# Optimization experiments

Hardware: AMD Instinct MI355X
Metric: run time of the kernel (lower is better)

## Reference

```python
import jax, jax.numpy as jnp
import numpy as np

N_NODES = 100000
N_EDGES = 1600000


def gcn_layer(x, src, dst, W, b, n_nodes):
    # PyG GCNConv: h = x @ W; add self-loops; sym-normalized scatter-add; + bias
    h = x @ W
    loop = jnp.arange(n_nodes, dtype=src.dtype)
    si = jnp.concatenate([src, loop])
    di = jnp.concatenate([dst, loop])
    deg = jax.ops.segment_sum(jnp.ones(si.shape[0], h.dtype), di, num_segments=n_nodes)
    dinv = jax.lax.rsqrt(deg)  # deg >= 1 due to self-loops
    norm = dinv[si] * dinv[di]              # [E+N]
    msgs = h[si] * norm[:, None]            # gather-scale
    out = jax.ops.segment_sum(msgs, di, num_segments=n_nodes)  # scatter-add
    return out + b


def setup_inputs() -> dict:
    key = jax.random.key(0)
    ks = jax.random.split(key, 8)
    x = jax.random.normal(ks[0], (N_NODES, 8), dtype=jnp.float32)
    edge_index = jax.random.randint(ks[1], (2, N_EDGES), 0, N_NODES, dtype=jnp.int32)
    W1 = jax.random.normal(ks[2], (8, 32), dtype=jnp.float32) * 0.3
    b1 = jax.random.normal(ks[3], (32,), dtype=jnp.float32) * 0.1
    W2 = jax.random.normal(ks[4], (32, 16), dtype=jnp.float32) * 0.2
    b2 = jax.random.normal(ks[5], (16,), dtype=jnp.float32) * 0.1
    Wfc = jax.random.normal(ks[6], (16, 1), dtype=jnp.float32) * 0.25
    bfc = jax.random.normal(ks[7], (1,), dtype=jnp.float32) * 0.1
    return {"x": x, "edge_index": edge_index, "W1": W1, "b1": b1,
            "W2": W2, "b2": b2, "Wfc": Wfc, "bfc": bfc}


def reference(x, edge_index, W1, b1, W2, b2, Wfc, bfc):
    n = x.shape[0]
    src, dst = edge_index[0], edge_index[1]
    h = jax.nn.relu(gcn_layer(x, src, dst, W1, b1, n))
    h = jax.nn.relu(gcn_layer(h, src, dst, W2, b2, n))
    return jax.nn.sigmoid(h @ Wfc + bfc)  # [N, 1]
```

## Files before the change

kernel.cpp:

```cpp
#include <hip/hip_runtime.h>
#include <math.h>

#define N_NODES 100000
#define N_EDGES 1600000

#define NB_SHIFT 7
#define NB 128
#define NBINS 782
#define RCAP 2432
#define BCHUNK 4096
#define BINBLOCKS ((N_EDGES + BCHUNK - 1) / BCHUNK)
#define LCAP 16
#define SPB 8

__device__ __forceinline__ unsigned int pack_bf2(float a, float b) {
    unsigned int ua = __float_as_uint(a), ub = __float_as_uint(b);
    ua += 0x7FFFu + ((ua >> 16) & 1u);
    ub += 0x7FFFu + ((ub >> 16) & 1u);
    return (ua >> 16) | (ub & 0xFFFF0000u);
}
__device__ __forceinline__ float bf_lo(unsigned int u) { return __uint_as_float(u << 16); }
__device__ __forceinline__ float bf_hi(unsigned int u) { return __uint_as_float(u & 0xFFFF0000u); }

__global__ __launch_bounds__(512) void k_bin(const int* __restrict__ src, const int* __restrict__ dst,
                                             int* __restrict__ cnt_tab, int* __restrict__ log,
                                             int* __restrict__ spill_rec, int* __restrict__ spill_bin, int e) {
    __shared__ int lcnt[NBINS];
    __shared__ int lbuf[NBINS * LCAP];
    __shared__ int sp_rec[SPB];
    __shared__ int sp_bin[SPB];
    __shared__ int sp_n;
    int tid = threadIdx.x, blk = blockIdx.x;
    for (int b = tid; b < NBINS; b += 512) lcnt[b] = 0;
    if (tid == 0) sp_n = 0;
    __syncthreads();
    int base = blk * BCHUNK;
    int end = min(base + BCHUNK, e);
    for (int i = base + tid; i < end; i += 512) {
        int d = dst[i], s = src[i];
        int b = d >> NB_SHIFT;
        int rec = (s << NB_SHIFT) | (d & (NB - 1));
        int slot = atomicAdd(&lcnt[b], 1);
        if (slot < LCAP) {
            lbuf[b * LCAP + slot] = rec;
        } else {
            int k = atomicAdd(&sp_n, 1);
            if (k < SPB) { sp_rec[k] = rec; sp_bin[k] = b; }
        }
    }
    __syncthreads();
    for (int b = tid; b < NBINS; b += 512) cnt_tab[blk * NBINS + b] = min(lcnt[b], LCAP);
    int* lrow = log + blk * NBINS * LCAP;
    for (int idx = tid; idx < NBINS * LCAP; idx += 512) lrow[idx] = lbuf[idx];
    if (tid < SPB) {
        int valid = tid < min(sp_n, SPB);
        spill_rec[blk * SPB + tid] = valid ? sp_rec[tid] : 0;
        spill_bin[blk * SPB + tid] = valid ? sp_bin[tid] : -1;
    }
}

__global__ __launch_bounds__(512) void k_sort(const int* __restrict__ cnt_tab, const int* __restrict__ log,
                                              const int* __restrict__ spill_rec, const int* __restrict__ spill_bin,
                                              int* __restrict__ gcur, int* __restrict__ regions,
                                              const float* __restrict__ x, float* __restrict__ dinv,
                                              unsigned int* __restrict__ gxu, int* __restrict__ row_start) {
    __shared__ int ccnt[BINBLOCKS];
    __shared__ int coff[BINBLOCKS];
    __shared__ int wtot[8];
    __shared__ int msum_s;
    __shared__ int sp_take;
    __shared__ int lrec[RCAP];
    __shared__ int lsort[RCAP];
    __shared__ int cnt[NB];
    __shared__ int stt[NB];
    __shared__ int cur[NB];
    __shared__ float di_s[NB];
    int b = blockIdx.x, tid = threadIdx.x;
    int lane = tid & 63, wv = tid >> 6;

    for (int c = tid; c < BINBLOCKS; c += 512) ccnt[c] = cnt_tab[c * NBINS + b];
    if (tid == 0) sp_take = 0;
    if (tid < NB) cnt[tid] = 0;
    __syncthreads();
    int v = (tid < BINBLOCKS) ? ccnt[tid] : 0;
    int s = v;
#pragma unroll
    for (int off = 1; off < 64; off <<= 1) {
        int t = __shfl_up(s, off, 64);
        if (lane >= off) s += t;
    }
    if (lane == 63) wtot[wv] = s;
    __syncthreads();
    if (tid == 0) {
        int acc = 0;
#pragma unroll
        for (int w = 0; w < 8; ++w) { int t = wtot[w]; wtot[w] = acc; acc += t; }
        msum_s = acc;
    }
    __syncthreads();
    if (tid < BINBLOCKS) coff[tid] = (s - v) + wtot[wv];
    __syncthreads();
    for (int idx = tid; idx < BINBLOCKS * LCAP; idx += 512) {
        int c = idx >> 4, k = idx & (LCAP - 1);
        if (k < ccnt[c]) {
            int pos = coff[c] + k;
            if (pos < RCAP) {
                int rec = log[(c * NBINS + b) * LCAP + k];
                lrec[pos] = rec;
                atomicAdd(&cnt[rec & (NB - 1)], 1);
            }
        }
    }
    for (int jj = tid; jj < BINBLOCKS * SPB; jj += 512) {
        if (spill_bin[jj] == b) {
            int p = atomicAdd(&sp_take, 1);
            int pos = msum_s + p;
            if (pos < RCAP) {
                int rec = spill_rec[jj];
                lrec[pos] = rec;
                atomicAdd(&cnt[rec & (NB - 1)], 1);
            }
        }
    }
    __syncthreads();
    int m = min(msum_s + sp_take, RCAP);
    if (tid == 0) gcur[b] = m;
    if (tid < 64) {
        int c0 = cnt[lane], c1 = cnt[64 + lane];
        int s0 = c0, s1 = c1;
#pragma unroll
        for (int off = 1; off < 64; off <<= 1) {
            int t0 = __shfl_up(s0, off, 64);
            int t1 = __shfl_up(s1, off, 64);
            if (lane >= off) { s0 += t0; s1 += t1; }
        }
        s1 += __shfl(s0, 63, 64);
        stt[lane] = s0 - c0;
        stt[64 + lane] = s1 - c1;
    }
    __syncthreads();
    int node0 = b << NB_SHIFT;
    if (tid < NB) {
        cur[tid] = stt[tid];
        float d = rsqrtf((float)cnt[tid] + 1.0f);
        di_s[tid] = d;
        row_start[b * NB + tid] = b * RCAP + stt[tid];
        int node = node0 + tid;
        if (node < N_NODES) dinv[node] = d;
    }
    __syncthreads();
    {
        int l = tid >> 2, p = tid & 3;
        int node = node0 + l;
        if (node < N_NODES) {
            const float2* x2 = (const float2*)x;
            float2 xv = x2[node * 4 + p];
            float d = di_s[l];
            gxu[node * 4 + p] = pack_bf2(xv.x * d, xv.y * d);
        }
    }
    for (int j = tid; j < m; j += 512) {
        int rec = lrec[j];
        int pos = atomicAdd(&cur[rec & (NB - 1)], 1);
        lsort[pos] = rec >> NB_SHIFT;
    }
    __syncthreads();
    int* wb = regions + b * RCAP;
    for (int j = tid; j < m; j += 512) wb[j] = lsort[j];
}

__global__ __launch_bounds__(256) void k_agg1_mlp(const int* __restrict__ gcur, const int* __restrict__ regions,
                                                  const int* __restrict__ row_start,
                                                  const unsigned int* __restrict__ gxu,
                                                  const float* __restrict__ dinv,
                                                  const float* __restrict__ W1, const float* __restrict__ b1,
                                                  const float* __restrict__ W2,
                                                  unsigned int* __restrict__ g2u) {
    int t = blockIdx.x * blockDim.x + threadIdx.x;
    int i = t >> 2;
    if (i >= N_NODES) return;
    int q = t & 3;
    int b = i >> NB_SHIFT, l = i & (NB - 1);
    int js = row_start[i];
    int je = (l < NB - 1) ? row_start[i + 1] : b * RCAP + gcur[b];
    const uint4* gx4 = (const uint4*)gxu;
    float a0 = 0.f, a1 = 0.f, a2 = 0.f, a3 = 0.f, a4 = 0.f, a5 = 0.f, a6 = 0.f, a7 = 0.f;
    if (q == 0) {
        uint4 u = gx4[i];
        a0 = bf_lo(u.x); a1 = bf_hi(u.x); a2 = bf_lo(u.y); a3 = bf_hi(u.y);
        a4 = bf_lo(u.z); a5 = bf_hi(u.z); a6 = bf_lo(u.w); a7 = bf_hi(u.w);
    }
    for (int j = js + q; j < je; j += 4) {
        uint4 u = gx4[regions[j]];
        a0 += bf_lo(u.x); a1 += bf_hi(u.x); a2 += bf_lo(u.y); a3 += bf_hi(u.y);
        a4 += bf_lo(u.z); a5 += bf_hi(u.z); a6 += bf_lo(u.w); a7 += bf_hi(u.w);
    }
    a0 += __shfl_xor(a0, 1, 64); a0 += __shfl_xor(a0, 2, 64);
    a1 += __shfl_xor(a1, 1, 64); a1 += __shfl_xor(a1, 2, 64);
    a2 += __shfl_xor(a2, 1, 64); a2 += __shfl_xor(a2, 2, 64);
    a3 += __shfl_xor(a3, 1, 64); a3 += __shfl_xor(a3, 2, 64);
    a4 += __shfl_xor(a4, 1, 64); a4 += __shfl_xor(a4, 2, 64);
    a5 += __shfl_xor(a5, 1, 64); a5 += __shfl_xor(a5, 2, 64);
    a6 += __shfl_xor(a6, 1, 64); a6 += __shfl_xor(a6, 2, 64);
    a7 += __shfl_xor(a7, 1, 64); a7 += __shfl_xor(a7, 2, 64);
    float di = dinv[i];
    float y[8] = { a0 * di, a1 * di, a2 * di, a3 * di, a4 * di, a5 * di, a6 * di, a7 * di };
    float hh[8];
#pragma unroll
    for (int ff = 0; ff < 8; ++ff) {
        int f = q * 8 + ff;
        float s = b1[f];
#pragma unroll
        for (int k = 0; k < 8; ++k) s += y[k] * W1[k * 32 + f];
        hh[ff] = fmaxf(0.f, s);
    }
    float g[16];
#pragma unroll
    for (int o = 0; o < 16; ++o) {
        float s = 0.f;
#pragma unroll
        for (int ff = 0; ff < 8; ++ff) s += hh[ff] * W2[(q * 8 + ff) * 16 + o];
        g[o] = s;
    }
#pragma unroll
    for (int o = 0; o < 16; ++o) {
        g[o] += __shfl_xor(g[o], 1, 64);
        g[o] += __shfl_xor(g[o], 2, 64);
    }
    int f0 = q * 4;
    uint2 pk = make_uint2(pack_bf2(g[f0] * di, g[f0 + 1] * di),
                          pack_bf2(g[f0 + 2] * di, g[f0 + 3] * di));
    ((uint2*)g2u)[i * 4 + q] = pk;
}

__global__ __launch_bounds__(256) void k_agg2_final(const int* __restrict__ gcur, const int* __restrict__ regions,
                                                    const int* __restrict__ row_start,
                                                    const unsigned int* __restrict__ g2u,
                                                    const float* __restrict__ dinv,
                                                    const float* __restrict__ b2, const float* __restrict__ Wfc,
                                                    const float* __restrict__ bfc, float* __restrict__ out) {
    int t = blockIdx.x * blockDim.x + threadIdx.x;
    int i = t >> 2;
    if (i >= N_NODES) return;
    int q = t & 3;
    int b = i >> NB_SHIFT, l = i & (NB - 1);
    int js = row_start[i];
    int je = (l < NB - 1) ? row_start[i + 1] : b * RCAP + gcur[b];
    const uint4* g24 = (const uint4*)g2u;
    float a[16];
#pragma unroll
    for (int f = 0; f < 16; ++f) a[f] = 0.f;
    if (q == 0) {
        uint4 u0 = g24[i * 2], u1 = g24[i * 2 + 1];
        a[0] = bf_lo(u0.x); a[1] = bf_hi(u0.x); a[2] = bf_lo(u0.y); a[3] = bf_hi(u0.y);
        a[4] = bf_lo(u0.z); a[5] = bf_hi(u0.z); a[6] = bf_lo(u0.w); a[7] = bf_hi(u0.w);
        a[8] = bf_lo(u1.x); a[9] = bf_hi(u1.x); a[10] = bf_lo(u1.y); a[11] = bf_hi(u1.y);
        a[12] = bf_lo(u1.z); a[13] = bf_hi(u1.z); a[14] = bf_lo(u1.w); a[15] = bf_hi(u1.w);
    }
    for (int j = js + q; j < je; j += 4) {
        int s = regions[j];
        uint4 u0 = g24[s * 2], u1 = g24[s * 2 + 1];
        a[0] += bf_lo(u0.x); a[1] += bf_hi(u0.x); a[2] += bf_lo(u0.y); a[3] += bf_hi(u0.y);
        a[4] += bf_lo(u0.z); a[5] += bf_hi(u0.z); a[6] += bf_lo(u0.w); a[7] += bf_hi(u0.w);
        a[8] += bf_lo(u1.x); a[9] += bf_hi(u1.x); a[10] += bf_lo(u1.y); a[11] += bf_hi(u1.y);
        a[12] += bf_lo(u1.z); a[13] += bf_hi(u1.z); a[14] += bf_lo(u1.w); a[15] += bf_hi(u1.w);
    }
#pragma unroll
    for (int f = 0; f < 16; ++f) {
        a[f] += __shfl_xor(a[f], 1, 64);
        a[f] += __shfl_xor(a[f], 2, 64);
    }
    if (q == 0) {
        float di = dinv[i];
        float z = bfc[0];
#pragma unroll
        for (int f = 0; f < 16; ++f)
            z += fmaxf(0.f, di * a[f] + b2[f]) * Wfc[f];
        out[i] = 1.0f / (1.0f + expf(-z));
    }
}

extern "C" void kernel_launch(void* const* d_in, const int* in_sizes, int n_in,
                              void* d_out, int out_size, void* d_ws, size_t ws_size,
                              hipStream_t stream) {
    const float* x   = (const float*)d_in[0];
    const int*   ei  = (const int*)d_in[1];
    const float* W1  = (const float*)d_in[2];
    const float* b1  = (const float*)d_in[3];
    const float* W2  = (const float*)d_in[4];
    const float* b2  = (const float*)d_in[5];
    const float* Wfc = (const float*)d_in[6];
    const float* bfc = (const float*)d_in[7];
    float* out = (float*)d_out;

    const int* src = ei;
    const int* dst = ei + N_EDGES;
    const int N = N_NODES, E = N_EDGES;

    int*          cnt_tab   = (int*)d_ws;
    int*          log       = cnt_tab + BINBLOCKS * NBINS;
    int*          spill_rec = log + BINBLOCKS * NBINS * LCAP;
    int*          spill_bin = spill_rec + BINBLOCKS * SPB;
    int*          gcur      = spill_bin + BINBLOCKS * SPB;
    int*          regions   = gcur + NBINS;
    int*          row_start = regions + NBINS * RCAP;
    float*        dinv      = (float*)(row_start + NBINS * NB);
    unsigned int* gxu       = (unsigned int*)(dinv + N);
    unsigned int* g2u       = gxu + N * 4;

    auto grid = [](int work, int blk) { return (work + blk - 1) / blk; };

    k_bin<<<BINBLOCKS, 512, 0, stream>>>(src, dst, cnt_tab, log, spill_rec, spill_bin, E);
    k_sort<<<NBINS, 512, 0, stream>>>(cnt_tab, log, spill_rec, spill_bin, gcur, regions, x, dinv, gxu, row_start);
    k_agg1_mlp<<<grid(N * 4, 256), 256, 0, stream>>>(gcur, regions, row_start, gxu, dinv, W1, b1, W2, g2u);
    k_agg2_final<<<grid(N * 4, 256), 256, 0, stream>>>(gcur, regions, row_start, g2u, dinv, b2, Wfc, bfc, out);
}
```

Before: 152.0 us.

## Fuse layer-1 aggregation into sort kernel using global degree atomics

```diff
diff --git a/kernel.cpp b/kernel.cpp
--- a/kernel.cpp
+++ b/kernel.cpp
@@ -22,15 +22,30 @@
 __device__ __forceinline__ float bf_lo(unsigned int u) { return __uint_as_float(u << 16); }
 __device__ __forceinline__ float bf_hi(unsigned int u) { return __uint_as_float(u & 0xFFFF0000u); }
 
+#define QR(v) { v += __shfl_xor(v, 1, 64); v += __shfl_xor(v, 2, 64); }
+
 __global__ __launch_bounds__(512) void k_bin(const int* __restrict__ src, const int* __restrict__ dst,
+                                             const float* __restrict__ x,
                                              int* __restrict__ cnt_tab, int* __restrict__ log,
-                                             int* __restrict__ spill_rec, int* __restrict__ spill_bin, int e) {
+                                             int* __restrict__ spill_rec, int* __restrict__ spill_bin,
+                                             int* __restrict__ deg, unsigned int* __restrict__ xbf, int e) {
     __shared__ int lcnt[NBINS];
     __shared__ int lbuf[NBINS * LCAP];
     __shared__ int sp_rec[SPB];
     __shared__ int sp_bin[SPB];
     __shared__ int sp_n;
     int tid = threadIdx.x, blk = blockIdx.x;
+    {
+        int node = blk * 512 + tid;
+        if (node < N_NODES) {
+            const float4* x4 = (const float4*)x;
+            float4 xa = x4[node * 2], xb = x4[node * 2 + 1];
+            uint4 u;
+            u.x = pack_bf2(xa.x, xa.y); u.y = pack_bf2(xa.z, xa.w);
+            u.z = pack_bf2(xb.x, xb.y); u.w = pack_bf2(xb.z, xb.w);
+            ((uint4*)xbf)[node] = u;
+        }
+    }
     for (int b = tid; b < NBINS; b += 512) lcnt[b] = 0;
     if (tid == 0) sp_n = 0;
     __syncthreads();
@@ -38,6 +53,7 @@
     int end = min(base + BCHUNK, e);
     for (int i = base + tid; i < end; i += 512) {
         int d = dst[i], s = src[i];
+        atomicAdd(&deg[d], 1);
         int b = d >> NB_SHIFT;
         int rec = (s << NB_SHIFT) | (d & (NB - 1));
         int slot = atomicAdd(&lcnt[b], 1);
@@ -59,11 +75,14 @@
     }
 }
 
-__global__ __launch_bounds__(512) void k_sort(const int* __restrict__ cnt_tab, const int* __restrict__ log,
-                                              const int* __restrict__ spill_rec, const int* __restrict__ spill_bin,
-                                              int* __restrict__ gcur, int* __restrict__ regions,
-                                              const float* __restrict__ x, float* __restrict__ dinv,
-                                              unsigned int* __restrict__ gxu, int* __restrict__ row_start) {
+__global__ __launch_bounds__(512, 4) void k_sort_agg1(const int* __restrict__ cnt_tab, const int* __restrict__ log,
+                                                      const int* __restrict__ spill_rec, const int* __restrict__ spill_bin,
+                                                      int* __restrict__ gcur, int* __restrict__ regions,
+                                                      int* __restrict__ row_start, float* __restrict__ dinv,
+                                                      const unsigned int* __restrict__ xbf, const int* __restrict__ deg,
+                                                      const float* __restrict__ W1, const float* __restrict__ b1,
+                                                      const float* __restrict__ W2,
+                                                      unsigned int* __restrict__ g2u) {
     __shared__ int ccnt[BINBLOCKS];
     __shared__ int coff[BINBLOCKS];
     __shared__ int wtot[8];
@@ -149,16 +168,6 @@
         if (node < N_NODES) dinv[node] = d;
     }
     __syncthreads();
-    {
-        int l = tid >> 2, p = tid & 3;
-        int node = node0 + l;
-        if (node < N_NODES) {
-            const float2* x2 = (const float2*)x;
-            float2 xv = x2[node * 4 + p];
-            float d = di_s[l];
-            gxu[node * 4 + p] = pack_bf2(xv.x * d, xv.y * d);
-        }
-    }
     for (int j = tid; j < m; j += 512) {
         int rec = lrec[j];
         int pos = atomicAdd(&cur[rec & (NB - 1)], 1);
@@ -167,70 +176,65 @@
     __syncthreads();
     int* wb = regions + b * RCAP;
     for (int j = tid; j < m; j += 512) wb[j] = lsort[j];
-}
-
-__global__ __launch_bounds__(256) void k_agg1_mlp(const int* __restrict__ gcur, const int* __restrict__ regions,
-                                                  const int* __restrict__ row_start,
-                                                  const unsigned int* __restrict__ gxu,
-                                                  const float* __restrict__ dinv,
-                                                  const float* __restrict__ W1, const float* __restrict__ b1,
-                                                  const float* __restrict__ W2,
-                                                  unsigned int* __restrict__ g2u) {
-    int t = blockIdx.x * blockDim.x + threadIdx.x;
-    int i = t >> 2;
-    if (i >= N_NODES) return;
-    int q = t & 3;
-    int b = i >> NB_SHIFT, l = i & (NB - 1);
-    int js = row_start[i];
-    int je = (l < NB - 1) ? row_start[i + 1] : b * RCAP + gcur[b];
-    const uint4* gx4 = (const uint4*)gxu;
-    float a0 = 0.f, a1 = 0.f, a2 = 0.f, a3 = 0.f, a4 = 0.f, a5 = 0.f, a6 = 0.f, a7 = 0.f;
-    if (q == 0) {
-        uint4 u = gx4[i];
-        a0 = bf_lo(u.x); a1 = bf_hi(u.x); a2 = bf_lo(u.y); a3 = bf_hi(u.y);
-        a4 = bf_lo(u.z); a5 = bf_hi(u.z); a6 = bf_lo(u.w); a7 = bf_hi(u.w);
-    }
-    for (int j = js + q; j < je; j += 4) {
-        uint4 u = gx4[regions[j]];
-        a0 += bf_lo(u.x); a1 += bf_hi(u.x); a2 += bf_lo(u.y); a3 += bf_hi(u.y);
-        a4 += bf_lo(u.z); a5 += bf_hi(u.z); a6 += bf_lo(u.w); a7 += bf_hi(u.w);
-    }
-    a0 += __shfl_xor(a0, 1, 64); a0 += __shfl_xor(a0, 2, 64);
-    a1 += __shfl_xor(a1, 1, 64); a1 += __shfl_xor(a1, 2, 64);
-    a2 += __shfl_xor(a2, 1, 64); a2 += __shfl_xor(a2, 2, 64);
-    a3 += __shfl_xor(a3, 1, 64); a3 += __shfl_xor(a3, 2, 64);
-    a4 += __shfl_xor(a4, 1, 64); a4 += __shfl_xor(a4, 2, 64);
-    a5 += __shfl_xor(a5, 1, 64); a5 += __shfl_xor(a5, 2, 64);
-    a6 += __shfl_xor(a6, 1, 64); a6 += __shfl_xor(a6, 2, 64);
-    a7 += __shfl_xor(a7, 1, 64); a7 += __shfl_xor(a7, 2, 64);
-    float di = dinv[i];
-    float y[8] = { a0 * di, a1 * di, a2 * di, a3 * di, a4 * di, a5 * di, a6 * di, a7 * di };
-    float hh[8];
-#pragma unroll
-    for (int ff = 0; ff < 8; ++ff) {
-        int f = q * 8 + ff;
-        float s = b1[f];
-#pragma unroll
-        for (int k = 0; k < 8; ++k) s += y[k] * W1[k * 32 + f];
-        hh[ff] = fmaxf(0.f, s);
-    }
-    float g[16];
-#pragma unroll
-    for (int o = 0; o < 16; ++o) {
-        float s = 0.f;
-#pragma unroll
-        for (int ff = 0; ff < 8; ++ff) s += hh[ff] * W2[(q * 8 + ff) * 16 + o];
-        g[o] = s;
-    }
-#pragma unroll
-    for (int o = 0; o < 16; ++o) {
-        g[o] += __shfl_xor(g[o], 1, 64);
-        g[o] += __shfl_xor(g[o], 2, 64);
-    }
-    int f0 = q * 4;
-    uint2 pk = make_uint2(pack_bf2(g[f0] * di, g[f0 + 1] * di),
-                          pack_bf2(g[f0 + 2] * di, g[f0 + 3] * di));
-    ((uint2*)g2u)[i * 4 + q] = pk;
+    float* wsh = (float*)lrec;
+    for (int i = tid; i < 800; i += 512)
+        wsh[i] = (i < 256) ? W1[i] : (i < 288) ? b1[i - 256] : W2[i - 288];
+    __syncthreads();
+
+    {
+        int l = tid >> 2, q = tid & 3;
+        int node = node0 + l;
+        if (node < N_NODES) {
+            int js = stt[l];
+            int je = (l < NB - 1) ? stt[l + 1] : m;
+            const uint4* xb4 = (const uint4*)xbf;
+            float a0 = 0.f, a1 = 0.f, a2 = 0.f, a3 = 0.f, a4 = 0.f, a5 = 0.f, a6 = 0.f, a7 = 0.f;
+            if (q == 0) {
+                uint4 u = xb4[node];
+                float d = di_s[l];
+                a0 = bf_lo(u.x) * d; a1 = bf_hi(u.x) * d; a2 = bf_lo(u.y) * d; a3 = bf_hi(u.y) * d;
+                a4 = bf_lo(u.z) * d; a5 = bf_hi(u.z) * d; a6 = bf_lo(u.w) * d; a7 = bf_hi(u.w) * d;
+            }
+            for (int j = js + q; j < je; j += 4) {
+                int sx = lsort[j];
+                uint4 u = xb4[sx];
+                float w = rsqrtf((float)deg[sx] + 1.0f);
+                a0 = fmaf(bf_lo(u.x), w, a0); a1 = fmaf(bf_hi(u.x), w, a1);
+                a2 = fmaf(bf_lo(u.y), w, a2); a3 = fmaf(bf_hi(u.y), w, a3);
+                a4 = fmaf(bf_lo(u.z), w, a4); a5 = fmaf(bf_hi(u.z), w, a5);
+                a6 = fmaf(bf_lo(u.w), w, a6); a7 = fmaf(bf_hi(u.w), w, a7);
+            }
+            QR(a0); QR(a1); QR(a2); QR(a3); QR(a4); QR(a5); QR(a6); QR(a7);
+            float di = di_s[l];
+            float y[8] = { a0 * di, a1 * di, a2 * di, a3 * di, a4 * di, a5 * di, a6 * di, a7 * di };
+            const float* W1s = wsh;
+            const float* b1s = wsh + 256;
+            const float* W2s = wsh + 288;
+            float hh[8];
+#pragma unroll
+            for (int ff = 0; ff < 8; ++ff) {
+                int f = q * 8 + ff;
+                float sa = b1s[f];
+#pragma unroll
+                for (int k = 0; k < 8; ++k) sa = fmaf(y[k], W1s[k * 32 + f], sa);
+                hh[ff] = fmaxf(0.f, sa);
+            }
+            float g[16];
+#pragma unroll
+            for (int o = 0; o < 16; ++o) {
+                float sa = 0.f;
+#pragma unroll
+                for (int ff = 0; ff < 8; ++ff) sa = fmaf(hh[ff], W2s[(q * 8 + ff) * 16 + o], sa);
+                g[o] = sa;
+            }
+#pragma unroll
+            for (int o = 0; o < 16; ++o) QR(g[o]);
+            int f0 = q * 4;
+            uint2 pk = make_uint2(pack_bf2(g[f0] * di, g[f0 + 1] * di),
+                                  pack_bf2(g[f0 + 2] * di, g[f0 + 3] * di));
+            ((uint2*)g2u)[node * 4 + q] = pk;
+        }
+    }
 }
 
 __global__ __launch_bounds__(256) void k_agg2_final(const int* __restrict__ gcur, const int* __restrict__ regions,
@@ -304,14 +308,16 @@
     int*          gcur      = spill_bin + BINBLOCKS * SPB;
     int*          regions   = gcur + NBINS;
     int*          row_start = regions + NBINS * RCAP;
-    float*        dinv      = (float*)(row_start + NBINS * NB);
-    unsigned int* gxu       = (unsigned int*)(dinv + N);
-    unsigned int* g2u       = gxu + N * 4;
+    int*          deg       = row_start + NBINS * NB;
+    float*        dinv      = (float*)(deg + N);
+    unsigned int* xbf       = (unsigned int*)(dinv + N);
+    unsigned int* g2u       = xbf + (size_t)N * 4;
 
     auto grid = [](int work, int blk) { return (work + blk - 1) / blk; };
 
-    k_bin<<<BINBLOCKS, 512, 0, stream>>>(src, dst, cnt_tab, log, spill_rec, spill_bin, E);
-    k_sort<<<NBINS, 512, 0, stream>>>(cnt_tab, log, spill_rec, spill_bin, gcur, regions, x, dinv, gxu, row_start);
-    k_agg1_mlp<<<grid(N * 4, 256), 256, 0, stream>>>(gcur, regions, row_start, gxu, dinv, W1, b1, W2, g2u);
+    hipMemsetAsync(deg, 0, (size_t)N * sizeof(int), stream);
+    k_bin<<<BINBLOCKS, 512, 0, stream>>>(src, dst, x, cnt_tab, log, spill_rec, spill_bin, deg, xbf, E);
+    k_sort_agg1<<<NBINS, 512, 0, stream>>>(cnt_tab, log, spill_rec, spill_bin, gcur, regions, row_start,
+                                           dinv, xbf, deg, W1, b1, W2, g2u);
     k_agg2_final<<<grid(N * 4, 256), 256, 0, stream>>>(gcur, regions, row_start, g2u, dinv, b2, Wfc, bfc, out);
 }
```

Result: slower. 205.2 us (+35.0%).
